# Kernel optimization log

Measured on AMD Instinct MI355X. Metric: run time of the kernel, lower is better.

## Reference

```python
import jax, jax.numpy as jnp
import numpy as np

DFL_CH = 16
NC = 20


def setup_inputs() -> dict:
    key = jax.random.key(0)
    k1, k2, k3, k4, k5 = jax.random.split(key, 5)
    b, h, w, c = 32, 80, 80, 128
    x = jax.random.normal(k1, (b, h, w, c), dtype=jnp.float32)
    w_box = jax.random.normal(k2, (c, 4 * DFL_CH), dtype=jnp.float32) * 0.05
    b_box = jax.random.normal(k3, (4 * DFL_CH,), dtype=jnp.float32) * 0.05
    w_cls = jax.random.normal(k4, (c, NC), dtype=jnp.float32) * 0.05
    b_cls = jax.random.normal(k5, (NC,), dtype=jnp.float32) * 0.05
    return {"x": x, "w_box": w_box, "b_box": b_box, "w_cls": w_cls,
            "b_cls": b_cls, "stride": 8}


def reference(x, w_box, b_box, w_cls, b_cls, stride):
    b, h, w, _ = x.shape
    hw = h * w
    # 1x1 convs == per-pixel matmuls (NHWC)
    box = jnp.einsum('bhwc,co->bhwo', x, w_box) + b_box   # [b,h,w,64]
    cls = jnp.einsum('bhwc,co->bhwo', x, w_cls) + b_cls   # [b,h,w,nc]
    cls_flat = cls.reshape(b, hw, NC)
    # DFL: softmax over 16 bins per coordinate, expectation with weights 0..15
    box_p = box.reshape(b, hw, 4, DFL_CH)
    probs = jax.nn.softmax(box_p, axis=-1)
    bins = jnp.arange(DFL_CH, dtype=x.dtype)
    box_dfl = jnp.einsum('bnfc,c->bnf', probs, bins)       # [b,hw,4]
    # anchor centers (tf.meshgrid default 'xy' indexing)
    s = jnp.asarray(stride, dtype=x.dtype)
    gx = (jnp.arange(w, dtype=x.dtype) + 0.5) * s
    gy = (jnp.arange(h, dtype=x.dtype) + 0.5) * s
    Gx, Gy = jnp.meshgrid(gx, gy)                          # each [h,w]
    anchors = jnp.stack([Gx, Gy], axis=-1).reshape(1, hw, 2)
    a = box_dfl[..., :2]
    bc = box_dfl[..., 2:]
    boxes = jnp.concatenate([(anchors - a + anchors + bc) * 0.5, bc - a], axis=-1)
    return jnp.concatenate([boxes, jax.nn.sigmoid(cls_flat)], axis=-1)
```

## Files before the change

kernel.cpp:

```cpp
#include <hip/hip_runtime.h>


typedef _Float16 half8 __attribute__((ext_vector_type(8)));
typedef __fp16  fp16x2 __attribute__((ext_vector_type(2)));
typedef float f32x4v __attribute__((ext_vector_type(4)));

constexpr int Cc = 128;
constexpr int NPAD = 96;
constexpr int WT_STRIDE = 136;
constexpr int NTILES = 6400;
constexpr int NWAVES = 2048;
constexpr float LOG2E = 1.44269504088896f;

union H8 { half8 h; fp16x2 p[4]; };

__device__ __forceinline__ float sigm(float v) {
    return __builtin_amdgcn_rcpf(1.f + __builtin_amdgcn_exp2f(-LOG2E * v));
}

__global__ __launch_bounds__(256, 2)
void head_kernel(const float* __restrict__ x,
                 const float* __restrict__ w_box,
                 const float* __restrict__ b_box,
                 const float* __restrict__ w_cls,
                 const float* __restrict__ b_cls,
                 const int*   __restrict__ stride_p,
                 float* __restrict__ out)
{
    __shared__ __align__(16) _Float16 Wt[NPAD][WT_STRIDE];
    __shared__ __align__(16) float bias_s[NPAD];
    __shared__ __align__(16) float sc[4][32][24];

    const int tid  = threadIdx.x;
    const int wave = tid >> 6;
    const int lane = tid & 63;
    const int c    = lane & 15;
    const int g    = lane >> 4;

    for (int i = tid; i < 128 * 16; i += 256) {
        int k   = i >> 4;
        int ch0 = (i & 15) << 2;
        int f   = ch0 >> 4;
        int b0  = ch0 & 15;
        int R0  = (b0 >> 2) * 16 + (f << 2);
        f32x4v v = *(const f32x4v*)&w_box[k * 64 + ch0];
        Wt[R0 + 0][k] = (_Float16)v[0];
        Wt[R0 + 1][k] = (_Float16)v[1];
        Wt[R0 + 2][k] = (_Float16)v[2];
        Wt[R0 + 3][k] = (_Float16)v[3];
    }
    for (int i = tid; i < 128 * 5; i += 256) {
        int k  = i / 5;
        int c4 = (i - k * 5) << 2;
        f32x4v v = *(const f32x4v*)&w_cls[k * 20 + c4];
        Wt[64 + c4 + 0][k] = (_Float16)v[0];
        Wt[64 + c4 + 1][k] = (_Float16)v[1];
        Wt[64 + c4 + 2][k] = (_Float16)v[2];
        Wt[64 + c4 + 3][k] = (_Float16)v[3];
    }
    for (int i = tid; i < 12 * 128; i += 256) {
        int ch = 84 + (i >> 7);
        int k  = i & 127;
        Wt[ch][k] = (_Float16)0.f;
    }
    if (tid < 64) {
        int f = tid >> 4, b = tid & 15;
        bias_s[(b >> 2) * 16 + (f << 2) + (b & 3)] = b_box[tid];
    } else if (tid < 96) {
        bias_s[tid] = (tid < 84) ? b_cls[tid - 64] : 0.f;
    }
    __syncthreads();

    const float sf = (float)stride_p[0];
    f32x4v bl[6];
    #pragma unroll
    for (int nt = 0; nt < 6; ++nt)
        bl[nt] = *(const f32x4v*)&bias_s[nt * 16 + g * 4];

    const int wid = blockIdx.x * 4 + wave;
    const int t0 = wid, t1 = wid + NWAVES, t2 = wid + 2 * NWAVES;
    const bool has4 = (wid & 7) == 0;
    const int t3 = 3 * NWAVES + (wid >> 3);

    f32x4v xvA[4][2][2], xvB[4][2][2];

    auto load_tile = [&](f32x4v (&xv)[4][2][2], int tile) {
        const float* xb = x + (size_t)(tile * 32 + c) * Cc + g * 8;
        #pragma unroll
        for (int ks = 0; ks < 4; ++ks)
            #pragma unroll
            for (int rt = 0; rt < 2; ++rt) {
                const float* p = xb + rt * 16 * Cc + ks * 32;
                xv[ks][rt][0] = *(const f32x4v*)p;
                xv[ks][rt][1] = *(const f32x4v*)(p + 4);
            }
        __builtin_amdgcn_sched_barrier(0);
    };

    auto compute_tile = [&](f32x4v (&xv)[4][2][2], int tile) {
        f32x4v acc[2][6];
        #pragma unroll
        for (int i = 0; i < 2; ++i)
            #pragma unroll
            for (int j = 0; j < 6; ++j)
                acc[i][j] = (f32x4v){0.f, 0.f, 0.f, 0.f};

        #pragma unroll
        for (int ks = 0; ks < 4; ++ks) {
            half8 wfrag[6];
            #pragma unroll
            for (int nt = 0; nt < 6; ++nt)
                wfrag[nt] = *(const half8*)&Wt[nt * 16 + c][ks * 32 + g * 8];
            #pragma unroll
            for (int rt = 0; rt < 2; ++rt) {
                f32x4v lo = xv[ks][rt][0], hi = xv[ks][rt][1];
                H8 bu;
                bu.p[0] = __builtin_amdgcn_cvt_pkrtz(lo[0], lo[1]);
                bu.p[1] = __builtin_amdgcn_cvt_pkrtz(lo[2], lo[3]);
                bu.p[2] = __builtin_amdgcn_cvt_pkrtz(hi[0], hi[1]);
                bu.p[3] = __builtin_amdgcn_cvt_pkrtz(hi[2], hi[3]);
                #pragma unroll
                for (int nt = 0; nt < 6; ++nt)
                    acc[rt][nt] = __builtin_amdgcn_mfma_f32_16x16x32_f16(wfrag[nt], bu.h, acc[rt][nt], 0, 0, 0);
            }
        }

        const int pos0 = (tile % 200) * 32;
        #pragma unroll
        for (int rt = 0; rt < 2; ++rt) {
            const int row = rt * 16 + c;
            float s = 0.f, ws = 0.f;
            #pragma unroll
            for (int t = 0; t < 4; ++t) {
                f32x4v v = acc[rt][t] + bl[t];
                float e0 = __builtin_amdgcn_exp2f(LOG2E * v[0]);
                float e1 = __builtin_amdgcn_exp2f(LOG2E * v[1]);
                float e2 = __builtin_amdgcn_exp2f(LOG2E * v[2]);
                float e3 = __builtin_amdgcn_exp2f(LOG2E * v[3]);
                s  += e0 + e1 + e2 + e3;
                ws += (float)(4 * t) * e0 + (float)(4 * t + 1) * e1
                    + (float)(4 * t + 2) * e2 + (float)(4 * t + 3) * e3;
            }
            const float dfl = ws * __builtin_amdgcn_rcpf(s);

            float* rp = sc[wave][row];
            rp[g] = dfl;
            f32x4v vA = acc[rt][4] + bl[4];
            f32x4v clsA = { sigm(vA[0]), sigm(vA[1]), sigm(vA[2]), sigm(vA[3]) };
            *(f32x4v*)(rp + 4 + 4 * g) = clsA;
            if (g == 0) {
                f32x4v vB = acc[rt][5] + bl[5];
                f32x4v clsB = { sigm(vB[0]), sigm(vB[1]), sigm(vB[2]), sigm(vB[3]) };
                *(f32x4v*)(rp + 20) = clsB;
            }
        }

        const float* s0 = &sc[wave][0][0];
        float* orow = out + (size_t)tile * 32 * 24;
        #pragma unroll
        for (int i = 0; i < 3; ++i) {
            const unsigned j = (unsigned)lane + 64u * i;
            f32x4v v = *(const f32x4v*)(s0 + j * 4);
            const unsigned row = j / 6u;
            if (j - 6u * row == 0u) {
                const unsigned pos = (unsigned)pos0 + row;
                const unsigned yp  = pos / 80u;
                const unsigned xq  = pos - 80u * yp;
                const float ax = ((float)xq + 0.5f) * sf;
                const float ay = ((float)yp + 0.5f) * sf;
                const float w2 = v[2] - v[0], w3 = v[3] - v[1];
                v = (f32x4v){ ax + 0.5f * w2, ay + 0.5f * w3, w2, w3 };
            }
            *(f32x4v*)(orow + j * 4) = v;
        }
    };

    load_tile(xvA, t0);
    load_tile(xvB, t1);
    compute_tile(xvA, t0);
    load_tile(xvA, t2);
    compute_tile(xvB, t1);
    if (has4) load_tile(xvB, t3);
    compute_tile(xvA, t2);
    if (has4) compute_tile(xvB, t3);
}

extern "C" void kernel_launch(void* const* d_in, const int* in_sizes, int n_in,
                              void* d_out, int out_size, void* d_ws, size_t ws_size,
                              hipStream_t stream) {
    const float* x      = (const float*)d_in[0];
    const float* w_box  = (const float*)d_in[1];
    const float* b_box  = (const float*)d_in[2];
    const float* w_cls  = (const float*)d_in[3];
    const float* b_cls  = (const float*)d_in[4];
    const int*   stride_p = (const int*)d_in[5];
    float* out = (float*)d_out;

    dim3 grid(512), block(256);
    hipLaunchKernelGGL(head_kernel, grid, block, 0, stream,
                       x, w_box, b_box, w_cls, b_cls, stride_p, out);
}
```

Measured before the change: 29.02 us.

## Use 16-row tiles with register-resident weights and finer load balancing

Cuts the per-wave tile from 32 to 16 rows, so each wave now handles 6 or 7 tiles instead of 3 or 4, which gives finer-grained load balance across waves. The weight fragments are loaded from LDS into registers once, instead of on every tile, and the bias is folded into the accumulator initialisation. This removes repeated LDS reads and lowers per-tile register pressure, at the cost of 24 persistent weight registers and more, smaller store phases with some idle lanes.

```diff
diff --git a/kernel.cpp b/kernel.cpp
--- a/kernel.cpp
+++ b/kernel.cpp
@@ -8,7 +8,6 @@
 constexpr int Cc = 128;
 constexpr int NPAD = 96;
 constexpr int WT_STRIDE = 136;
-constexpr int NTILES = 6400;
 constexpr int NWAVES = 2048;
 constexpr float LOG2E = 1.44269504088896f;
 
@@ -29,7 +28,7 @@
 {
     __shared__ __align__(16) _Float16 Wt[NPAD][WT_STRIDE];
     __shared__ __align__(16) float bias_s[NPAD];
-    __shared__ __align__(16) float sc[4][32][24];
+    __shared__ __align__(16) float sc[4][16][24];
 
     const int tid  = threadIdx.x;
     const int wave = tid >> 6;
@@ -71,118 +70,111 @@
     }
     __syncthreads();
 
+    half8 wf[4][6];
+    #pragma unroll
+    for (int ks = 0; ks < 4; ++ks)
+        #pragma unroll
+        for (int nt = 0; nt < 6; ++nt)
+            wf[ks][nt] = *(const half8*)&Wt[nt * 16 + c][ks * 32 + g * 8];
+
     const float sf = (float)stride_p[0];
-    f32x4v bl[6];
-    #pragma unroll
-    for (int nt = 0; nt < 6; ++nt)
-        bl[nt] = *(const f32x4v*)&bias_s[nt * 16 + g * 4];
 
     const int wid = blockIdx.x * 4 + wave;
-    const int t0 = wid, t1 = wid + NWAVES, t2 = wid + 2 * NWAVES;
-    const bool has4 = (wid & 7) == 0;
-    const int t3 = 3 * NWAVES + (wid >> 3);
+    const bool heavy = (wave == (blockIdx.x & 3));
+    const int t6 = 6 * NWAVES + blockIdx.x;
 
-    f32x4v xvA[4][2][2], xvB[4][2][2];
+    f32x4v xvA[4][2], xvB[4][2];
 
-    auto load_tile = [&](f32x4v (&xv)[4][2][2], int tile) {
-        const float* xb = x + (size_t)(tile * 32 + c) * Cc + g * 8;
+    auto load_tile = [&](f32x4v (&xv)[4][2], int tile) {
+        const float* xb = x + (size_t)(tile * 16 + c) * Cc + g * 8;
         #pragma unroll
-        for (int ks = 0; ks < 4; ++ks)
-            #pragma unroll
-            for (int rt = 0; rt < 2; ++rt) {
-                const float* p = xb + rt * 16 * Cc + ks * 32;
-                xv[ks][rt][0] = *(const f32x4v*)p;
-                xv[ks][rt][1] = *(const f32x4v*)(p + 4);
-            }
+        for (int ks = 0; ks < 4; ++ks) {
+            const float* p = xb + ks * 32;
+            xv[ks][0] = *(const f32x4v*)p;
+            xv[ks][1] = *(const f32x4v*)(p + 4);
+        }
         __builtin_amdgcn_sched_barrier(0);
     };
 
-    auto compute_tile = [&](f32x4v (&xv)[4][2][2], int tile) {
-        f32x4v acc[2][6];
+    auto compute_tile = [&](f32x4v (&xv)[4][2], int tile) {
+        f32x4v acc[6];
         #pragma unroll
-        for (int i = 0; i < 2; ++i)
-            #pragma unroll
-            for (int j = 0; j < 6; ++j)
-                acc[i][j] = (f32x4v){0.f, 0.f, 0.f, 0.f};
+        for (int nt = 0; nt < 6; ++nt)
+            acc[nt] = *(const f32x4v*)&bias_s[nt * 16 + g * 4];
 
         #pragma unroll
         for (int ks = 0; ks < 4; ++ks) {
-            half8 wfrag[6];
+            f32x4v lo = xv[ks][0], hi = xv[ks][1];
+            H8 bu;
+            bu.p[0] = __builtin_amdgcn_cvt_pkrtz(lo[0], lo[1]);
+            bu.p[1] = __builtin_amdgcn_cvt_pkrtz(lo[2], lo[3]);
+            bu.p[2] = __builtin_amdgcn_cvt_pkrtz(hi[0], hi[1]);
+            bu.p[3] = __builtin_amdgcn_cvt_pkrtz(hi[2], hi[3]);
             #pragma unroll
             for (int nt = 0; nt < 6; ++nt)
-                wfrag[nt] = *(const half8*)&Wt[nt * 16 + c][ks * 32 + g * 8];
-            #pragma unroll
-            for (int rt = 0; rt < 2; ++rt) {
-                f32x4v lo = xv[ks][rt][0], hi = xv[ks][rt][1];
-                H8 bu;
-                bu.p[0] = __builtin_amdgcn_cvt_pkrtz(lo[0], lo[1]);
-                bu.p[1] = __builtin_amdgcn_cvt_pkrtz(lo[2], lo[3]);
-                bu.p[2] = __builtin_amdgcn_cvt_pkrtz(hi[0], hi[1]);
-                bu.p[3] = __builtin_amdgcn_cvt_pkrtz(hi[2], hi[3]);
-                #pragma unroll
-                for (int nt = 0; nt < 6; ++nt)
-                    acc[rt][nt] = __builtin_amdgcn_mfma_f32_16x16x32_f16(wfrag[nt], bu.h, acc[rt][nt], 0, 0, 0);
-            }
+                acc[nt] = __builtin_amdgcn_mfma_f32_16x16x32_f16(wf[ks][nt], bu.h, acc[nt], 0, 0, 0);
         }
 
-        const int pos0 = (tile % 200) * 32;
+        const int pos0 = (tile % 400) * 16;
+
+        float s = 0.f, ws = 0.f;
         #pragma unroll
-        for (int rt = 0; rt < 2; ++rt) {
-            const int row = rt * 16 + c;
-            float s = 0.f, ws = 0.f;
-            #pragma unroll
-            for (int t = 0; t < 4; ++t) {
-                f32x4v v = acc[rt][t] + bl[t];
-                float e0 = __builtin_amdgcn_exp2f(LOG2E * v[0]);
-                float e1 = __builtin_amdgcn_exp2f(LOG2E * v[1]);
-                float e2 = __builtin_amdgcn_exp2f(LOG2E * v[2]);
-                float e3 = __builtin_amdgcn_exp2f(LOG2E * v[3]);
-                s  += e0 + e1 + e2 + e3;
-                ws += (float)(4 * t) * e0 + (float)(4 * t + 1) * e1
-                    + (float)(4 * t + 2) * e2 + (float)(4 * t + 3) * e3;
-            }
-            const float dfl = ws * __builtin_amdgcn_rcpf(s);
+        for (int t = 0; t < 4; ++t) {
+            f32x4v v = acc[t];
+            float e0 = __builtin_amdgcn_exp2f(LOG2E * v[0]);
+            float e1 = __builtin_amdgcn_exp2f(LOG2E * v[1]);
+            float e2 = __builtin_amdgcn_exp2f(LOG2E * v[2]);
+            float e3 = __builtin_amdgcn_exp2f(LOG2E * v[3]);
+            s  += e0 + e1 + e2 + e3;
+            ws += (float)(4 * t) * e0 + (float)(4 * t + 1) * e1
+                + (float)(4 * t + 2) * e2 + (float)(4 * t + 3) * e3;
+        }
+        const float dfl = ws * __builtin_amdgcn_rcpf(s);
 
-            float* rp = sc[wave][row];
-            rp[g] = dfl;
-            f32x4v vA = acc[rt][4] + bl[4];
-            f32x4v clsA = { sigm(vA[0]), sigm(vA[1]), sigm(vA[2]), sigm(vA[3]) };
-            *(f32x4v*)(rp + 4 + 4 * g) = clsA;
-            if (g == 0) {
-                f32x4v vB = acc[rt][5] + bl[5];
-                f32x4v clsB = { sigm(vB[0]), sigm(vB[1]), sigm(vB[2]), sigm(vB[3]) };
-                *(f32x4v*)(rp + 20) = clsB;
-            }
+        float* rp = sc[wave][c];
+        rp[g] = dfl;
+        f32x4v clsA = { sigm(acc[4][0]), sigm(acc[4][1]), sigm(acc[4][2]), sigm(acc[4][3]) };
+        *(f32x4v*)(rp + 4 + 4 * g) = clsA;
+        if (g == 0) {
+            f32x4v clsB = { sigm(acc[5][0]), sigm(acc[5][1]), sigm(acc[5][2]), sigm(acc[5][3]) };
+            *(f32x4v*)(rp + 20) = clsB;
         }
 
         const float* s0 = &sc[wave][0][0];
-        float* orow = out + (size_t)tile * 32 * 24;
+        float* orow = out + (size_t)tile * (16 * 24);
         #pragma unroll
-        for (int i = 0; i < 3; ++i) {
-            const unsigned j = (unsigned)lane + 64u * i;
-            f32x4v v = *(const f32x4v*)(s0 + j * 4);
-            const unsigned row = j / 6u;
-            if (j - 6u * row == 0u) {
-                const unsigned pos = (unsigned)pos0 + row;
-                const unsigned yp  = pos / 80u;
-                const unsigned xq  = pos - 80u * yp;
-                const float ax = ((float)xq + 0.5f) * sf;
-                const float ay = ((float)yp + 0.5f) * sf;
-                const float w2 = v[2] - v[0], w3 = v[3] - v[1];
-                v = (f32x4v){ ax + 0.5f * w2, ay + 0.5f * w3, w2, w3 };
+        for (int i = 0; i < 2; ++i) {
+            const int j = lane + 64 * i;
+            if (j < 96) {
+                f32x4v v = *(const f32x4v*)(s0 + j * 4);
+                const int row = j / 6;
+                if (j - 6 * row == 0) {
+                    const int pos = pos0 + row;
+                    const int yp  = pos / 80;
+                    const int xq  = pos - 80 * yp;
+                    const float ax = ((float)xq + 0.5f) * sf;
+                    const float ay = ((float)yp + 0.5f) * sf;
+                    const float w2 = v[2] - v[0], w3 = v[3] - v[1];
+                    v = (f32x4v){ ax + 0.5f * w2, ay + 0.5f * w3, w2, w3 };
+                }
+                *(f32x4v*)(orow + j * 4) = v;
             }
-            *(f32x4v*)(orow + j * 4) = v;
         }
     };
 
+    const int t0 = wid,              t1 = wid + NWAVES;
+    const int t2 = wid + 2 * NWAVES, t3 = wid + 3 * NWAVES;
+    const int t4 = wid + 4 * NWAVES, t5 = wid + 5 * NWAVES;
+
     load_tile(xvA, t0);
     load_tile(xvB, t1);
-    compute_tile(xvA, t0);
-    load_tile(xvA, t2);
-    compute_tile(xvB, t1);
-    if (has4) load_tile(xvB, t3);
-    compute_tile(xvA, t2);
-    if (has4) compute_tile(xvB, t3);
+    compute_tile(xvA, t0);  load_tile(xvA, t2);
+    compute_tile(xvB, t1);  load_tile(xvB, t3);
+    compute_tile(xvA, t2);  load_tile(xvA, t4);
+    compute_tile(xvB, t3);  load_tile(xvB, t5);
+    compute_tile(xvA, t4);  if (heavy) load_tile(xvA, t6);
+    compute_tile(xvB, t5);
+    if (heavy) compute_tile(xvA, t6);
 }
 
 extern "C" void kernel_launch(void* const* d_in, const int* in_sizes, int n_in,
```

Result: no change. 28.47 us (-1.9%).
